# Optimization experiments

Measured on AMD Instinct MI355X. Metric: run time of the kernel, lower is better.

## Reference

```python
import jax, jax.numpy as jnp
import numpy as np

B, C, H, W = 4, 288, 64, 64
P = 2
HEADS = 36
MLP_RATIO = 4.0
D = C * P * P              # hidden_size = 1152
HF = int(D * MLP_RATIO)    # 4608
LN_EPS = 1e-6
ATTN_EPS = 1e-8


def _layernorm(x):
    # LayerNorm over [C,H,W] per sample, no affine
    mu = jnp.mean(x, axis=(1, 2, 3), keepdims=True)
    var = jnp.mean((x - mu) ** 2, axis=(1, 2, 3), keepdims=True)
    return (x - mu) * jax.lax.rsqrt(var + LN_EPS)


def _seg(x):
    # b c (n1 p) (n2 p) -> b (n1 n2) (c p p)
    b, c, h, w = x.shape
    n1, n2 = h // P, w // P
    x = x.reshape(b, c, n1, P, n2, P).transpose(0, 2, 4, 1, 3, 5)
    return x.reshape(b, n1 * n2, c * P * P)


def _comb(t, h, w):
    # b (n1 n2) (c p p) -> b c (n1 p) (n2 p)
    b, n, dd = t.shape
    n1, n2 = h // P, w // P
    c = dd // (P * P)
    x = t.reshape(b, n1, n2, c, P, P).transpose(0, 3, 1, 4, 2, 5)
    return x.reshape(b, c, h, w)


def _lite_la(t, qkv_w, proj_w, proj_b):
    # ReLU-kernel linear attention with ones-padding normalization trick
    b, s, dm = t.shape
    d = dm // HEADS
    qkv = t @ qkv_w.T                       # [b,s,3*dm]
    q, k, v = jnp.split(qkv, 3, axis=-1)
    q = jax.nn.relu(q).reshape(b, s, HEADS, d)
    k = jax.nn.relu(k).reshape(b, s, HEADS, d)
    v = v.reshape(b, s, HEADS, d)
    v = jnp.concatenate([v, jnp.ones((b, s, HEADS, 1), v.dtype)], axis=-1)  # PAD_VAL=1
    vk = jnp.einsum('bshe,bshd->bhed', v, k)       # [b,h,d+1,d]
    out = jnp.einsum('bhed,bshd->bshe', vk, q)     # [b,s,h,d+1]
    out = out[..., :-1] / (out[..., -1:] + ATTN_EPS)
    return out.reshape(b, s, dm) @ proj_w.T + proj_b


def _glumb(t, inv_w, inv_b, dw_w, dw_b, pw_w):
    # GLU MBConv: 1x1 expand + SiLU -> 3x3 depthwise -> GLU gate -> 1x1 project
    b, n, c = t.shape
    hp = wp = int(n ** 0.5)
    x = t.reshape(b, hp, wp, c).transpose(0, 3, 1, 2)  # NCHW
    x = jnp.einsum('bchw,oc->bohw', x, inv_w[:, :, 0, 0]) + inv_b[None, :, None, None]
    x = jax.nn.silu(x)
    x = jax.lax.conv_general_dilated(x, dw_w, (1, 1), 'SAME',
                                     feature_group_count=dw_w.shape[0],
                                     dimension_numbers=('NCHW', 'OIHW', 'NCHW'))
    x = x + dw_b[None, :, None, None]
    x, gate = jnp.split(x, 2, axis=1)
    x = x * jax.nn.silu(gate)
    x = jnp.einsum('bchw,oc->bohw', x, pw_w[:, :, 0, 0])
    return x.reshape(b, c, n).transpose(0, 2, 1)


def setup_inputs() -> dict:
    key = jax.random.key(0)
    ks = jax.random.split(key, 10)
    s = 0.02
    return {
        'x': jax.random.normal(ks[0], (B, C, H, W), jnp.float32),
        'cond': jax.random.normal(ks[1], (B, 6 * C, H, W), jnp.float32),
        'global_token': jax.random.normal(ks[2], (B, D), jnp.float32),
        'time_token': jax.random.normal(ks[3], (B, D), jnp.float32),
        'ss_w': jax.random.normal(ks[4], (6 * C, 6 * C, 1, 1), jnp.float32) * s,
        'ss_b': jnp.zeros((6 * C,), jnp.float32),
        'qkv_w': jax.random.normal(ks[5], (3 * D, D), jnp.float32) * s,
        'proj_w': jax.random.normal(ks[6], (D, D), jnp.float32) * s,
        'proj_b': jnp.zeros((D,), jnp.float32),
        'inv_w': jax.random.normal(ks[7], (2 * HF, D, 1, 1), jnp.float32) * s,
        'inv_b': jnp.zeros((2 * HF,), jnp.float32),
        'dw_w': jax.random.normal(ks[8], (2 * HF, 1, 3, 3), jnp.float32) * s,
        'dw_b': jnp.zeros((2 * HF,), jnp.float32),
        'pw_w': jax.random.normal(ks[9], (D, HF, 1, 1), jnp.float32) * s,
    }


def reference(x, cond, global_token, time_token, ss_w, ss_b, qkv_w, proj_w, proj_b,
              inv_w, inv_b, dw_w, dw_b, pw_w):
    # scale_shift_table: SiLU + 1x1 conv on cond, chunk into 6 per-channel maps
    ss = jnp.einsum('bchw,oc->bohw', jax.nn.silu(cond), ss_w[:, :, 0, 0]) + ss_b[None, :, None, None]
    sh_msa, sc_msa, g_msa, sh_mlp, sc_mlp, g_mlp = jnp.split(ss, 6, axis=1)
    # attention branch
    tok = _seg(_layernorm(x) * (1.0 + sc_msa) + sh_msa)
    tok = jnp.concatenate([global_token[:, None], time_token[:, None], tok], axis=1)
    a = _lite_la(tok, qkv_w, proj_w, proj_b)
    x = x + _comb(a[:, 2:], H, W) * g_msa
    # MLP branch
    m = _glumb(_seg(_layernorm(x) * (1.0 + sc_mlp) + sh_mlp), inv_w, inv_b, dw_w, dw_b, pw_w)
    x = x + _comb(m, H, W) * g_mlp
    return x
```

## Files before the change

kernel.cpp:

```cpp
#include <hip/hip_runtime.h>
#include <hip/hip_bf16.h>
#include <cstdint>


typedef __bf16 bf16;
typedef bf16 bf16x8 __attribute__((ext_vector_type(8)));
typedef bf16 bf16x4 __attribute__((ext_vector_type(4)));
typedef float f32x4 __attribute__((ext_vector_type(4)));

typedef const __attribute__((address_space(1))) void gas_void;
typedef __attribute__((address_space(3))) void las_void;

__device__ __forceinline__ void gload16(const bf16* g, bf16* l) {
    __builtin_amdgcn_global_load_lds((gas_void*)g, (las_void*)l, 16, 0, 0);
}

#define BB 4
#define CC 288
#define HW 4096
#define C6 1728
#define DD 1152
#define SEQ 1026
#define RTOT 4104
#define NTOK 1024
#define HF 4608
#define HF2 9216
#define NPB 1179648

static constexpr size_t OFF_SUMS = 0;
static constexpr size_t OFF_SS   = 256;
static constexpr size_t SS_BYTES = (size_t)C6 * 16384 * 2;
static constexpr size_t OFF_R2   = OFF_SS + SS_BYTES;
static constexpr size_t OFF_PART1= OFF_R2;
static constexpr size_t OFF_A1   = OFF_R2;
static constexpr size_t OFF_T    = OFF_R2;
static constexpr size_t OFF_QKV  = OFF_T   + (size_t)RTOT*DD*2;
static constexpr size_t OFF_PART2= OFF_QKV;
static constexpr size_t OFF_VK   = OFF_QKV + (size_t)3456*RTOT*2;
static constexpr size_t OFF_ATT  = OFF_VK  + (size_t)144*1056*4;
static constexpr size_t OFF_APROJ= OFF_ATT + (size_t)RTOT*DD*2;
static constexpr size_t OFF_T2   = OFF_R2;
static constexpr size_t OFF_Y    = OFF_T2  + (size_t)4096*DD*2;
static constexpr size_t OFF_G    = OFF_Y   + (size_t)4096*HF2*2;
static constexpr size_t OFF_M    = OFF_G   + (size_t)4096*HF*2;
static constexpr size_t OFF_W    = OFF_R2  + 132120576;
static constexpr size_t OFF_WSS  = OFF_W;
static constexpr size_t OFF_WQKV = OFF_WSS  + (size_t)C6*C6*2;
static constexpr size_t OFF_WPROJ= OFF_WQKV + (size_t)3456*DD*2;
static constexpr size_t OFF_WINV = OFF_WPROJ+ (size_t)DD*DD*2;
static constexpr size_t OFF_WPW  = OFF_WINV + (size_t)HF2*DD*2;

__global__ __launch_bounds__(256) void cvt_bf16(const float* __restrict__ s,
                                                bf16* __restrict__ d, int n4) {
    int i = blockIdx.x * 256 + threadIdx.x;
    if (i < n4) {
        float4 v = ((const float4*)s)[i];
        bf16x4 o = {(bf16)v.x, (bf16)v.y, (bf16)v.z, (bf16)v.w};
        ((bf16x4*)d)[i] = o;
    }
}

__device__ __forceinline__ void block_reduce2_store(float s1, float s2, float* dst) {
    #pragma unroll
    for (int o = 32; o > 0; o >>= 1) { s1 += __shfl_down(s1, o); s2 += __shfl_down(s2, o); }
    __shared__ float r1[4], r2[4];
    int wave = threadIdx.x >> 6, lane = threadIdx.x & 63;
    if (lane == 0) { r1[wave] = s1; r2[wave] = s2; }
    __syncthreads();
    if (threadIdx.x == 0) {
        dst[0] = r1[0] + r1[1] + r1[2] + r1[3];
        dst[1] = r2[0] + r2[1] + r2[2] + r2[3];
    }
}

__global__ __launch_bounds__(256) void ln_stats(const float* __restrict__ x, float* __restrict__ part) {
    const float* base = x + (size_t)blockIdx.x * 4096;
    float s1 = 0.f, s2 = 0.f;
    #pragma unroll
    for (int it = 0; it < 4; it++) {
        float4 v = ((const float4*)base)[it * 256 + threadIdx.x];
        s1 += v.x + v.y + v.z + v.w;
        s2 += v.x * v.x + v.y * v.y + v.z * v.z + v.w * v.w;
    }
    block_reduce2_store(s1, s2, part + (size_t)blockIdx.x * 2);
}

__global__ __launch_bounds__(256) void reduce_part(const float* __restrict__ part, float* __restrict__ sums,
                                                   int nper, int out_off) {
    int b = blockIdx.x;
    float s1 = 0.f, s2 = 0.f;
    for (int i = threadIdx.x; i < nper; i += 256) {
        s1 += part[(size_t)(b * nper + i) * 2];
        s2 += part[(size_t)(b * nper + i) * 2 + 1];
    }
    block_reduce2_store(s1, s2, sums + out_off + b * 2);
}

__global__ __launch_bounds__(256) void prep_cond(const float* __restrict__ cond, bf16* __restrict__ A1) {
    __shared__ float tile[64][65];
    int b = blockIdx.z, k0 = blockIdx.y * 64, h0 = blockIdx.x * 64;
    int col = threadIdx.x & 63, r4 = threadIdx.x >> 6;
    const float* src = cond + ((size_t)b * C6 + k0) * HW + h0;
    #pragma unroll
    for (int p = 0; p < 16; p++) {
        int kk = r4 + p * 4;
        float v = src[(size_t)kk * HW + col];
        tile[col][kk] = v / (1.f + __expf(-v));
    }
    __syncthreads();
    bf16* dst = A1 + ((size_t)(b * HW + h0)) * C6 + k0;
    #pragma unroll
    for (int p = 0; p < 16; p++) {
        int rr = r4 + p * 4;
        dst[(size_t)rr * C6 + col] = (bf16)tile[rr][col];
    }
}

template <int EP, int BIAS>
__global__ __launch_bounds__(256) void gemm_bt(const bf16* __restrict__ A, const bf16* __restrict__ B,
                                               const float* __restrict__ bias, bf16* __restrict__ C,
                                               int M, int N, int K, int reluLimit) {
    __shared__ __align__(16) bf16 As[128 * 32];
    __shared__ __align__(16) bf16 Bs[128 * 32];
    const int tid = threadIdx.x, wave = tid >> 6, lane = tid & 63;

    const int nx = gridDim.x, ny = gridDim.y, G = 8;
    int idx = blockIdx.y * nx + blockIdx.x;
    int total = nx * ny;
    int q = total >> 3, rm = total & 7;
    int xcd = idx & 7, slot = idx >> 3;
    int vid = (xcd < rm ? xcd * (q + 1) : rm * (q + 1) + (xcd - rm) * q) + slot;
    int band = vid / (G * nx);
    int r = vid - band * (G * nx);
    int gm = min(G, ny - band * G);
    const int m0 = (band * G + r % gm) * 128;
    const int n0 = (r / gm) * 128;

    const int c0 = wave * 128 + lane;
    const int c1 = c0 + 64;
    const int sw = ((c0 >> 2) & 3) ^ ((c0 >> 4) & 3);
    const int ka = (((c0 & 3) ^ sw)) * 8;
    int ra0 = min(m0 + (c0 >> 2), M - 1), ra1 = min(m0 + (c1 >> 2), M - 1);
    int rb0 = min(n0 + (c0 >> 2), N - 1), rb1 = min(n0 + (c1 >> 2), N - 1);
    const bf16* gA0 = A + (size_t)ra0 * K + ka;
    const bf16* gA1 = A + (size_t)ra1 * K + ka;
    const bf16* gB0 = B + (size_t)rb0 * K + ka;
    const bf16* gB1 = B + (size_t)rb1 * K + ka;
    bf16* lA0 = As + wave * 1024;
    bf16* lA1 = As + wave * 1024 + 512;
    bf16* lB0 = Bs + wave * 1024;
    bf16* lB1 = Bs + wave * 1024 + 512;

    const int wm = (wave >> 1) * 64, wn = (wave & 1) * 64;
    const int l15 = lane & 15;
    const int sr = (l15 & 3) ^ ((l15 >> 2) & 3);
    const int fc = ((lane >> 4) ^ sr) * 8;
    const bf16* fa = As + (wm + l15) * 32 + fc;
    const bf16* fb = Bs + (wn + l15) * 32 + fc;

    f32x4 acc[4][4];
    #pragma unroll
    for (int i = 0; i < 4; i++)
        #pragma unroll
        for (int j = 0; j < 4; j++) acc[i][j] = (f32x4){0.f, 0.f, 0.f, 0.f};

    for (int kt = 0; kt < K; kt += 32) {
        __syncthreads();
        gload16(gA0, lA0); gload16(gA1, lA1);
        gload16(gB0, lB0); gload16(gB1, lB1);
        gA0 += 32; gA1 += 32; gB0 += 32; gB1 += 32;
        __syncthreads();
        bf16x8 af[4], bv[4];
        #pragma unroll
        for (int i = 0; i < 4; i++) af[i] = *(const bf16x8*)(fa + i * 16 * 32);
        #pragma unroll
        for (int j = 0; j < 4; j++) bv[j] = *(const bf16x8*)(fb + j * 16 * 32);
        #pragma unroll
        for (int i = 0; i < 4; i++)
            #pragma unroll
            for (int j = 0; j < 4; j++)
                acc[i][j] = __builtin_amdgcn_mfma_f32_16x16x32_bf16(af[i], bv[j], acc[i][j], 0, 0, 0);
    }

    const int mq = (lane >> 4) * 4, nl = lane & 15;
    #pragma unroll
    for (int i = 0; i < 4; i++) {
        #pragma unroll
        for (int j = 0; j < 4; j++) {
            int n = n0 + wn + j * 16 + nl;
            if (n < N) {
                #pragma unroll
                for (int r2 = 0; r2 < 4; r2++) {
                    int m = m0 + wm + i * 16 + mq + r2;
                    if (m < M) {
                        float v = acc[i][j][r2];
                        if (BIAS == 1) v += bias[m];
                        else if (BIAS == 2) v += bias[n];
                        if (EP == 1) { if (m < reluLimit) v = fmaxf(v, 0.f); }
                        else if (EP == 2) { v = v / (1.f + __expf(-v)); }
                        C[(size_t)m * N + n] = (bf16)v;
                    }
                }
            }
        }
    }
}

__global__ __launch_bounds__(256) void build_tok_t(const float* __restrict__ xs, const bf16* __restrict__ ss,
                                                   const float* __restrict__ sums, int soff, int shb, int scb,
                                                   bf16* __restrict__ dst, int tokoff, int seqstride) {
    __shared__ bf16 tl[32][132];
    int cch = blockIdx.x, n1 = blockIdx.y, b = blockIdx.z;
    int c0 = cch * 32;
    int tid = threadIdx.x, cl = tid >> 3, wseg = tid & 7;

    float mu = sums[soff + b * 2] * (1.f / (float)NPB);
    float var = sums[soff + b * 2 + 1] * (1.f / (float)NPB) - mu * mu;
    float rsig = rsqrtf(var + 1e-6f);

    int c = c0 + cl;
    #pragma unroll
    for (int hh = 0; hh < 2; hh++) {
        int hw = (2 * n1 + hh) * 64 + wseg * 8;
        const float* xp = xs + ((size_t)b * CC + c) * HW + hw;
        float4 x0 = ((const float4*)xp)[0];
        float4 x1 = ((const float4*)xp)[1];
        bf16x8 scv = *(const bf16x8*)(ss + (size_t)(scb + c) * 16384 + b * HW + hw);
        bf16x8 shv = *(const bf16x8*)(ss + (size_t)(shb + c) * 16384 + b * HW + hw);
        float xv[8] = {x0.x, x0.y, x0.z, x0.w, x1.x, x1.y, x1.z, x1.w};
        #pragma unroll
        for (int k = 0; k < 8; k++) {
            int w = wseg * 8 + k;
            float v = (xv[k] - mu) * rsig * (1.f + (float)scv[k]) + (float)shv[k];
            tl[w >> 1][cl * 4 + hh * 2 + (w & 1)] = (bf16)v;
        }
    }
    __syncthreads();
    int token = tid >> 3, seg = (tid & 7) * 16;
    bf16* drow = dst + ((size_t)(b * seqstride + tokoff + n1 * 32 + token)) * DD + c0 * 4 + seg;
    *(bf16x8*)drow = *(const bf16x8*)&tl[token][seg];
    *(bf16x8*)(drow + 8) = *(const bf16x8*)&tl[token][seg + 8];
}

__global__ __launch_bounds__(256) void copy_gt(const float* __restrict__ gtok, const float* __restrict__ ttok,
                                               bf16* __restrict__ T) {
    int which = blockIdx.x, b = blockIdx.y;
    const float* src = (which == 0 ? gtok : ttok) + b * DD;
    bf16* dst = T + (size_t)(b * SEQ + which) * DD;
    for (int d = threadIdx.x; d < DD; d += 256) dst[d] = (bf16)src[d];
}

__global__ __launch_bounds__(256) void attn_vk(const bf16* __restrict__ qkv, float* __restrict__ vk) {
    int bh = blockIdx.x >> 2, sb = blockIdx.x & 3;
    int b = bh / 36, h = bh % 36;
    int s_begin = sb * 288;
    int s_end = min(s_begin + 288, SEQ);
    const bf16* kbase = qkv + (size_t)(DD + h * 32) * RTOT + b * SEQ;
    const bf16* vbase = qkv + (size_t)(2 * DD + h * 32) * RTOT + b * SEQ;
    __shared__ __align__(16) bf16 kk[32][80];
    __shared__ __align__(16) bf16 vv[32][80];
    int tid = threadIdx.x;
    int e = tid >> 3, dg = (tid & 7) * 4;
    int lrow = tid >> 3, lcol = (tid & 7) * 8;
    float a0 = 0.f, a1 = 0.f, a2 = 0.f, a3 = 0.f, aD = 0.f;
    for (int s0 = s_begin; s0 < s_end; s0 += 64) {
        __syncthreads();
        #pragma unroll
        for (int j = 0; j < 8; j++) {
            int s = s0 + lcol + j;
            bool ok = s < s_end;
            kk[lrow][lcol + j] = ok ? kbase[(size_t)lrow * RTOT + s] : (bf16)0.f;
            vv[lrow][lcol + j] = ok ? vbase[(size_t)lrow * RTOT + s] : (bf16)0.f;
        }
        __syncthreads();
        #pragma unroll
        for (int j0 = 0; j0 < 64; j0 += 8) {
            bf16x8 vvv = *(const bf16x8*)&vv[e][j0];
            bf16x8 k0 = *(const bf16x8*)&kk[dg + 0][j0];
            bf16x8 k1 = *(const bf16x8*)&kk[dg + 1][j0];
            bf16x8 k2 = *(const bf16x8*)&kk[dg + 2][j0];
            bf16x8 k3 = *(const bf16x8*)&kk[dg + 3][j0];
            #pragma unroll
            for (int j = 0; j < 8; j++) {
                float vf = (float)vvv[j];
                a0 += vf * (float)k0[j];
                a1 += vf * (float)k1[j];
                a2 += vf * (float)k2[j];
                a3 += vf * (float)k3[j];
            }
            if (tid < 32) {
                bf16x8 kd = *(const bf16x8*)&kk[tid][j0];
                #pragma unroll
                for (int j = 0; j < 8; j++) aD += (float)kd[j];
            }
        }
    }
    float* dst = vk + (size_t)bh * 1056;
    atomicAdd(&dst[e * 32 + dg + 0], a0);
    atomicAdd(&dst[e * 32 + dg + 1], a1);
    atomicAdd(&dst[e * 32 + dg + 2], a2);
    atomicAdd(&dst[e * 32 + dg + 3], a3);
    if (tid < 32) atomicAdd(&dst[1024 + tid], aD);
}

__global__ __launch_bounds__(256) void attn_out(const bf16* __restrict__ qkv, const float* __restrict__ vk,
                                                bf16* __restrict__ att) {
    int bh = blockIdx.y, b = bh / 36, h = bh % 36;
    int s0 = blockIdx.x * 64;
    __shared__ float vks[1056];
    __shared__ __align__(16) bf16 qs[32][80];
    int tid = threadIdx.x;
    for (int i = tid; i < 1056; i += 256) vks[i] = vk[(size_t)bh * 1056 + i];
    const bf16* qbase = qkv + (size_t)(h * 32) * RTOT + b * SEQ;
    int lrow = tid >> 3, lcol = (tid & 7) * 8;
    #pragma unroll
    for (int j = 0; j < 8; j++) {
        int s = s0 + lcol + j;
        qs[lrow][lcol + j] = (s < SEQ) ? qbase[(size_t)lrow * RTOT + s] : (bf16)0.f;
    }
    __syncthreads();
    int sl = tid >> 2, eg = (tid & 3) * 8;
    int s = s0 + sl;
    float num[8] = {0.f, 0.f, 0.f, 0.f, 0.f, 0.f, 0.f, 0.f};
    float den = 0.f;
    #pragma unroll
    for (int d = 0; d < 32; d++) {
        float qv = (float)qs[d][sl];
        den += vks[1024 + d] * qv;
        #pragma unroll
        for (int t = 0; t < 8; t++) num[t] += vks[(eg + t) * 32 + d] * qv;
    }
    if (s < SEQ) {
        float inv = 1.f / (den + 1e-8f);
        bf16* dst = att + ((size_t)(b * SEQ + s)) * DD + h * 32 + eg;
        #pragma unroll
        for (int t = 0; t < 8; t++) dst[t] = (bf16)(num[t] * inv);
    }
}

__global__ __launch_bounds__(256) void add_attn(const float* __restrict__ x, const bf16* __restrict__ aproj,
                                                const bf16* __restrict__ ss, float* __restrict__ xo,
                                                float* __restrict__ part) {
    int b = blockIdx.x / 4608;
    size_t idx = (size_t)blockIdx.x * 256 + threadIdx.x;
    size_t local = idx - (size_t)b * NPB;
    int c = (int)(local >> 12), hw = (int)(local & 4095);
    int hh = hw >> 6, w = hw & 63;
    int n = (hh >> 1) * 32 + (w >> 1);
    int dd = c * 4 + (hh & 1) * 2 + (w & 1);
    float a = (float)aproj[(size_t)dd * RTOT + b * SEQ + 2 + n];
    float g = (float)ss[(size_t)(576 + c) * 16384 + b * HW + hw];
    float v = x[idx] + a * g;
    xo[idx] = v;
    block_reduce2_store(v, v * v, part + (size_t)blockIdx.x * 2);
}

__global__ __launch_bounds__(256) void dwglu(const bf16* __restrict__ y, const float* __restrict__ dw_w,
                                             const float* __restrict__ dw_b, bf16* __restrict__ g) {
    __shared__ __align__(16) bf16 xs[6400];
    __shared__ __align__(16) bf16 gs[6400];
    int b = blockIdx.z, tile = blockIdx.y, c0 = blockIdx.x * 64;
    int ty = (tile >> 2) * 8, tx = (tile & 3) * 8;
    int tid = threadIdx.x, cc = tid & 63, pg = tid >> 6;
    for (int p = pg; p < 100; p += 4) {
        int py = ty + p / 10 - 1, px = tx + p % 10 - 1;
        bool in = (py >= 0 && py < 32 && px >= 0 && px < 32);
        size_t base = ((size_t)(b * NTOK + py * 32 + px)) * HF2;
        xs[p * 64 + cc] = in ? y[base + c0 + cc] : (bf16)0.f;
        gs[p * 64 + cc] = in ? y[base + HF + c0 + cc] : (bf16)0.f;
    }
    float wx[9], wg[9];
    #pragma unroll
    for (int t = 0; t < 9; t++) {
        wx[t] = dw_w[(size_t)(c0 + cc) * 9 + t];
        wg[t] = dw_w[(size_t)(HF + c0 + cc) * 9 + t];
    }
    float bx = dw_b[c0 + cc], bg = dw_b[HF + c0 + cc];
    __syncthreads();
    for (int p = pg * 16; p < pg * 16 + 16; p++) {
        int py = p >> 3, px = p & 7;
        float ax = bx, ag = bg;
        #pragma unroll
        for (int dy = 0; dy < 3; dy++)
            #pragma unroll
            for (int dx = 0; dx < 3; dx++) {
                int q = (py + dy) * 10 + (px + dx);
                ax += (float)xs[q * 64 + cc] * wx[dy * 3 + dx];
                ag += (float)gs[q * 64 + cc] * wg[dy * 3 + dx];
            }
        float out = ax * (ag / (1.f + __expf(-ag)));
        g[((size_t)(b * NTOK + (ty + py) * 32 + tx + px)) * HF + c0 + cc] = (bf16)out;
    }
}

__global__ __launch_bounds__(256) void add_mlp(const bf16* __restrict__ mm, const bf16* __restrict__ ss,
                                               float* __restrict__ xo) {
    int b = blockIdx.x / 4608;
    size_t idx = (size_t)blockIdx.x * 256 + threadIdx.x;
    size_t local = idx - (size_t)b * NPB;
    int c = (int)(local >> 12), hw = (int)(local & 4095);
    int hh = hw >> 6, w = hw & 63;
    int n = (hh >> 1) * 32 + (w >> 1);
    int dd = c * 4 + (hh & 1) * 2 + (w & 1);
    float mv = (float)mm[(size_t)dd * 4096 + b * NTOK + n];
    float g = (float)ss[(size_t)(1440 + c) * 16384 + b * HW + hw];
    xo[idx] = xo[idx] + mv * g;
}

extern "C" void kernel_launch(void* const* d_in, const int* in_sizes, int n_in,
                              void* d_out, int out_size, void* d_ws, size_t ws_size,
                              hipStream_t stream) {
    (void)in_sizes; (void)n_in; (void)out_size; (void)ws_size;
    const float* x      = (const float*)d_in[0];
    const float* cond   = (const float*)d_in[1];
    const float* gtok   = (const float*)d_in[2];
    const float* ttok   = (const float*)d_in[3];
    const float* ss_w   = (const float*)d_in[4];
    const float* ss_b   = (const float*)d_in[5];
    const float* qkv_w  = (const float*)d_in[6];
    const float* proj_w = (const float*)d_in[7];
    const float* proj_b = (const float*)d_in[8];
    const float* inv_w  = (const float*)d_in[9];
    const float* inv_b  = (const float*)d_in[10];
    const float* dw_w   = (const float*)d_in[11];
    const float* dw_b   = (const float*)d_in[12];
    const float* pw_w   = (const float*)d_in[13];
    float* out = (float*)d_out;
    char* ws = (char*)d_ws;

    float* sums  = (float*)(ws + OFF_SUMS);
    float* PART1 = (float*)(ws + OFF_PART1);
    float* PART2 = (float*)(ws + OFF_PART2);
    bf16* SS    = (bf16*)(ws + OFF_SS);
    bf16* A1    = (bf16*)(ws + OFF_A1);
    bf16* T     = (bf16*)(ws + OFF_T);
    bf16* QKV   = (bf16*)(ws + OFF_QKV);
    float* VK   = (float*)(ws + OFF_VK);
    bf16* ATT   = (bf16*)(ws + OFF_ATT);
    bf16* APROJ = (bf16*)(ws + OFF_APROJ);
    bf16* T2    = (bf16*)(ws + OFF_T2);
    bf16* Y     = (bf16*)(ws + OFF_Y);
    bf16* G     = (bf16*)(ws + OFF_G);
    bf16* MM    = (bf16*)(ws + OFF_M);
    bf16* WSS   = (bf16*)(ws + OFF_WSS);
    bf16* WQKV  = (bf16*)(ws + OFF_WQKV);
    bf16* WPROJ = (bf16*)(ws + OFF_WPROJ);
    bf16* WINV  = (bf16*)(ws + OFF_WINV);
    bf16* WPW   = (bf16*)(ws + OFF_WPW);

    cvt_bf16<<<2916, 256, 0, stream>>>(ss_w, WSS, C6 * C6 / 4);
    cvt_bf16<<<3888, 256, 0, stream>>>(qkv_w, WQKV, 3456 * DD / 4);
    cvt_bf16<<<1296, 256, 0, stream>>>(proj_w, WPROJ, DD * DD / 4);
    cvt_bf16<<<10368, 256, 0, stream>>>(inv_w, WINV, HF2 * DD / 4);
    cvt_bf16<<<5184, 256, 0, stream>>>(pw_w, WPW, DD * HF / 4);

    ln_stats<<<1152, 256, 0, stream>>>(x, PART1);
    reduce_part<<<4, 256, 0, stream>>>(PART1, sums, 288, 0);
    prep_cond<<<dim3(64, 27, 4), 256, 0, stream>>>(cond, A1);
    gemm_bt<0, 1><<<dim3(128, 14), 256, 0, stream>>>(WSS, A1, ss_b, SS, C6, 16384, C6, 0);
    build_tok_t<<<dim3(9, 32, 4), 256, 0, stream>>>(x, SS, sums, 0, 0, 288, T, 2, SEQ);
    copy_gt<<<dim3(2, 4), 256, 0, stream>>>(gtok, ttok, T);
    gemm_bt<1, 0><<<dim3(33, 27), 256, 0, stream>>>(WQKV, T, nullptr, QKV, 3456, RTOT, DD, 2304);
    hipMemsetAsync(ws + OFF_VK, 0, (size_t)144 * 1056 * 4, stream);
    attn_vk<<<576, 256, 0, stream>>>(QKV, VK);
    attn_out<<<dim3(17, 144), 256, 0, stream>>>(QKV, VK, ATT);
    gemm_bt<0, 1><<<dim3(33, 9), 256, 0, stream>>>(WPROJ, ATT, proj_b, APROJ, DD, RTOT, DD, 0);
    add_attn<<<18432, 256, 0, stream>>>(x, APROJ, SS, out, PART2);
    reduce_part<<<4, 256, 0, stream>>>(PART2, sums, 4608, 8);
    build_tok_t<<<dim3(9, 32, 4), 256, 0, stream>>>(out, SS, sums, 8, 864, 1152, T2, 0, 1024);
    gemm_bt<2, 2><<<dim3(72, 32), 256, 0, stream>>>(T2, WINV, inv_b, Y, 4096, HF2, DD, 0);
    dwglu<<<dim3(72, 16, 4), 256, 0, stream>>>(Y, dw_w, dw_b, G);
    gemm_bt<0, 0><<<dim3(32, 9), 256, 0, stream>>>(WPW, G, nullptr, MM, DD, 4096, HF, 0);
    add_mlp<<<18432, 256, 0, stream>>>(MM, SS, out);
}
```

Baseline: 1.040 ms.

## Double-buffer GEMM LDS tiles to overlap global loads with MFMA

Splits the GEMM shared-memory tiles into two buffers and restructures the K loop so the next tile's global-to-LDS loads are issued before computing on the current tile, using explicit vmcnt waits and barriers. This hides global memory latency behind MFMA work instead of serializing load and compute. It doubles LDS use per block, which may reduce occupancy, and assumes an even tile count along K.

```diff
diff --git a/kernel.cpp b/kernel.cpp
--- a/kernel.cpp
+++ b/kernel.cpp
@@ -120,8 +120,8 @@
 __global__ __launch_bounds__(256) void gemm_bt(const bf16* __restrict__ A, const bf16* __restrict__ B,
                                                const float* __restrict__ bias, bf16* __restrict__ C,
                                                int M, int N, int K, int reluLimit) {
-    __shared__ __align__(16) bf16 As[128 * 32];
-    __shared__ __align__(16) bf16 Bs[128 * 32];
+    __shared__ __align__(16) bf16 As[2][128 * 32];
+    __shared__ __align__(16) bf16 Bs[2][128 * 32];
     const int tid = threadIdx.x, wave = tid >> 6, lane = tid & 63;
 
     const int nx = gridDim.x, ny = gridDim.y, G = 8;
@@ -146,17 +146,14 @@
     const bf16* gA1 = A + (size_t)ra1 * K + ka;
     const bf16* gB0 = B + (size_t)rb0 * K + ka;
     const bf16* gB1 = B + (size_t)rb1 * K + ka;
-    bf16* lA0 = As + wave * 1024;
-    bf16* lA1 = As + wave * 1024 + 512;
-    bf16* lB0 = Bs + wave * 1024;
-    bf16* lB1 = Bs + wave * 1024 + 512;
 
     const int wm = (wave >> 1) * 64, wn = (wave & 1) * 64;
     const int l15 = lane & 15;
     const int sr = (l15 & 3) ^ ((l15 >> 2) & 3);
     const int fc = ((lane >> 4) ^ sr) * 8;
-    const bf16* fa = As + (wm + l15) * 32 + fc;
-    const bf16* fb = Bs + (wn + l15) * 32 + fc;
+    const int fao = (wm + l15) * 32 + fc;
+    const int fbo = (wn + l15) * 32 + fc;
+    const int lwo = wave * 1024;
 
     f32x4 acc[4][4];
     #pragma unroll
@@ -164,12 +161,16 @@
         #pragma unroll
         for (int j = 0; j < 4; j++) acc[i][j] = (f32x4){0.f, 0.f, 0.f, 0.f};
 
-    for (int kt = 0; kt < K; kt += 32) {
-        __syncthreads();
-        gload16(gA0, lA0); gload16(gA1, lA1);
-        gload16(gB0, lB0); gload16(gB1, lB1);
+    auto STAGE = [&](int buf) {
+        gload16(gA0, &As[buf][lwo]);
+        gload16(gA1, &As[buf][lwo + 512]);
+        gload16(gB0, &Bs[buf][lwo]);
+        gload16(gB1, &Bs[buf][lwo + 512]);
         gA0 += 32; gA1 += 32; gB0 += 32; gB1 += 32;
-        __syncthreads();
+    };
+    auto COMP = [&](int buf) {
+        const bf16* fa = &As[buf][fao];
+        const bf16* fb = &Bs[buf][fbo];
         bf16x8 af[4], bv[4];
         #pragma unroll
         for (int i = 0; i < 4; i++) af[i] = *(const bf16x8*)(fa + i * 16 * 32);
@@ -180,7 +181,36 @@
             #pragma unroll
             for (int j = 0; j < 4; j++)
                 acc[i][j] = __builtin_amdgcn_mfma_f32_16x16x32_bf16(af[i], bv[j], acc[i][j], 0, 0, 0);
-    }
+    };
+
+    const int nt = K >> 5;
+    STAGE(0);
+    for (int it = 0; it < (nt >> 1) - 1; ++it) {
+        STAGE(1);
+        asm volatile("s_waitcnt vmcnt(4)" ::: "memory");
+        __builtin_amdgcn_s_barrier();
+        asm volatile("" ::: "memory");
+        COMP(0);
+        asm volatile("" ::: "memory");
+        __builtin_amdgcn_s_barrier();
+        STAGE(0);
+        asm volatile("s_waitcnt vmcnt(4)" ::: "memory");
+        __builtin_amdgcn_s_barrier();
+        asm volatile("" ::: "memory");
+        COMP(1);
+        asm volatile("" ::: "memory");
+        __builtin_amdgcn_s_barrier();
+    }
+    STAGE(1);
+    asm volatile("s_waitcnt vmcnt(4)" ::: "memory");
+    __builtin_amdgcn_s_barrier();
+    asm volatile("" ::: "memory");
+    COMP(0);
+    asm volatile("" ::: "memory");
+    asm volatile("s_waitcnt vmcnt(0)" ::: "memory");
+    __builtin_amdgcn_s_barrier();
+    asm volatile("" ::: "memory");
+    COMP(1);
 
     const int mq = (lane >> 4) * 4, nl = lane & 15;
     #pragma unroll
```

Measured after the change: 964.6 us. 1.08x faster.
